# Performance work log

Hardware: AMD Instinct MI355X
Metric: run time of the kernel (lower is better)

Reference implementation:

```python
import jax, jax.numpy as jnp
import numpy as np

B = 64          # batch of puzzles
N = 16          # board_size
H = 128         # hidden_dim
S = 3           # msg_passing_steps
E = 131072      # edges per edge type
T = 5           # edge types: contains, lt, gt, may_contain, diff
NCELL = B * N * N          # 16384 cell nodes
NCLU = B * (N + 1)         # 1088 cluster nodes


def setup_inputs() -> dict:
    key = jax.random.key(0)
    ks = jax.random.split(key, 20)
    # edges[t] = (src, dst). Type 0 ('contains') sources from cluster nodes,
    # the rest are cell-to-cell. Destinations are always cell nodes.
    src0 = jax.random.randint(ks[0], (1, E), 0, NCLU)
    srcr = jax.random.randint(ks[1], (T - 1, E), 0, NCELL)
    src = jnp.concatenate([src0, srcr], axis=0)
    dst = jax.random.randint(ks[2], (T, E), 0, NCELL)
    edges = jnp.stack([src, dst], axis=1).astype(jnp.int32)  # [T,2,E]
    q = jax.random.randint(ks[3], (NCELL,), 0, N + 1).astype(jnp.int32)

    def lin(k, fan_in, shape):
        return (jax.random.normal(k, shape, dtype=jnp.float32) / np.sqrt(fan_in)).astype(jnp.float32)

    inp = {
        'edges': edges,
        'q': q,
        'input_embeddings': lin(ks[4], H, (NCLU, H)) * np.sqrt(H) * 0.1,
        'output_embeddings': lin(ks[5], H, (NCLU, H)) * np.sqrt(H) * 0.1,
        'mlp_W1': lin(ks[6], 2 * H, (T, 2 * H, H)),
        'mlp_b1': jnp.zeros((T, H), jnp.float32),
        'mlp_W2': lin(ks[7], H, (T, H, H)),
        'mlp_b2': jnp.zeros((T, H), jnp.float32),
        'mlp_W3': lin(ks[8], H, (T, H, H)),
        'mlp_b3': jnp.zeros((T, H), jnp.float32),
        'mlp_W4': lin(ks[9], H, (T, H, H)),
        'mlp_b4': jnp.zeros((T, H), jnp.float32),
        'lstm_Wih': lin(ks[10], (T + 1) * H, ((T + 1) * H, 4 * H)),
        'lstm_Whh': lin(ks[11], H, (H, 4 * H)),
    }
    return inp


def _forward(edges, q, input_embeddings, output_embeddings,
             mlp_W1, mlp_b1, mlp_W2, mlp_b2, mlp_W3, mlp_b3, mlp_W4, mlp_b4,
             lstm_Wih, lstm_Whh):
    cell_sno = jnp.arange(NCELL, dtype=jnp.int32) // (N * N)
    clu_sno = jnp.arange(NCLU, dtype=jnp.int32) // (N + 1)
    clu_id = jnp.arange(NCLU, dtype=jnp.int32) % (N + 1)

    # cluster input: embedding lookup at id + (N+1)*sno
    cluster_x = input_embeddings[clu_id + (N + 1) * clu_sno]  # [NCLU, H]

    # cell input: class-0 row replaced by mean of classes 1..N, then lookup by q
    emb = input_embeddings.reshape(B, N + 1, H)
    avg = emb[:, 1:, :].mean(axis=1, keepdims=True)
    lookup = jnp.concatenate([avg, emb[:, 1:, :]], axis=1).reshape(NCLU, H)
    cell_x = lookup[q + (N + 1) * cell_sno]  # [NCELL, H]

    h = cell_x
    rnn_h = jnp.zeros_like(cell_x)
    rnn_c = jnp.zeros_like(cell_x)
    h_clu = cluster_x  # cluster state held fixed across steps

    outs = []
    for _ in range(S):
        msgs = []
        for t in range(T):
            src, dst = edges[t, 0], edges[t, 1]
            hs = (h_clu if t == 0 else h)[src]   # gather source states
            hd = h[dst]                           # gather dest states
            z = jnp.concatenate([hs, hd], axis=-1)          # [E, 2H]
            z = jax.nn.relu(z @ mlp_W1[t] + mlp_b1[t])
            z = jax.nn.relu(z @ mlp_W2[t] + mlp_b2[t])
            z = jax.nn.relu(z @ mlp_W3[t] + mlp_b3[t])
            z = z @ mlp_W4[t] + mlp_b4[t]                   # final Linear, no ReLU
            msgs.append(jax.ops.segment_sum(z, dst, num_segments=NCELL))
        lstm_in = jnp.concatenate([cell_x] + msgs, axis=-1)  # [NCELL, (T+1)H]
        gates = lstm_in @ lstm_Wih + rnn_h @ lstm_Whh        # bias=False LSTMCell
        i, f, g, o = jnp.split(gates, 4, axis=-1)            # torch gate order
        rnn_c = jax.nn.sigmoid(f) * rnn_c + jax.nn.sigmoid(i) * jnp.tanh(g)
        rnn_h = jax.nn.sigmoid(o) * jnp.tanh(rnn_c)
        h = rnn_h
        outs.append(h)

    cell_outputs = jnp.stack(outs)  # [S, NCELL, H]
    # calc_logits: bilinear contraction of cell states with output class embeddings
    logits = jnp.einsum('sbnh,bch->sbnc',
                        cell_outputs.reshape(S, B, N * N, H),
                        output_embeddings.reshape(B, N + 1, H))
    return logits.reshape(S, B * N * N, N + 1)


def reference(edges, q, input_embeddings, output_embeddings,
              mlp_W1, mlp_b1, mlp_W2, mlp_b2, mlp_W3, mlp_b3, mlp_W4, mlp_b4,
              lstm_Wih, lstm_Whh):
    return _forward(edges, q, input_embeddings, output_embeddings,
                    mlp_W1, mlp_b1, mlp_W2, mlp_b2, mlp_W3, mlp_b3, mlp_W4, mlp_b4,
                    lstm_Wih, lstm_Whh)
```

## Files before the change

kernel.cpp:

```cpp
#include <hip/hip_runtime.h>
#include <hip/hip_fp16.h>
#include <math.h>

#define H 128
#define SSTEPS 3
#define NE 131072
#define NT 5
#define NCELL 16384
#define NCLU 1088
#define G4 512
#define MSGW 640
#define AKT 28
#define EB 128

typedef unsigned short u16;
typedef unsigned int u32;
typedef __attribute__((ext_vector_type(8))) short short8;
typedef __attribute__((ext_vector_type(8))) unsigned short ushort8;
typedef __attribute__((ext_vector_type(4))) unsigned short ushort4v;
typedef __attribute__((ext_vector_type(4))) float f32x4;

__device__ __forceinline__ u16 f2bf(float f) {
    unsigned int u = __float_as_uint(f);
    u += 0x7fffu + ((u >> 16) & 1u);
    return (u16)(u >> 16);
}
__device__ __forceinline__ float bf2f(u16 h) {
    return __uint_as_float(((unsigned int)h) << 16);
}

__global__ __launch_bounds__(128) void k_avg(const float* __restrict__ emb,
                                             float* __restrict__ avg) {
    int b = blockIdx.x, hc = threadIdx.x;
    float s = 0.f;
#pragma unroll
    for (int r = 1; r <= 16; ++r) s += emb[(b * 17 + r) * H + hc];
    avg[b * H + hc] = s * (1.0f / 16.0f);
}

__global__ __launch_bounds__(256) void k_init(const int* __restrict__ q,
                                              const float* __restrict__ emb,
                                              const float* __restrict__ avg,
                                              u16* __restrict__ Ap, size_t aplane,
                                              float* __restrict__ rnn_h,
                                              float* __restrict__ cst) {
    __shared__ float sx[16][132];
    int mtile = blockIdx.x, tid = threadIdx.x;
#pragma unroll
    for (int e = 0; e < 8; ++e) {
        int idx = e * 256 + tid;
        int row = idx >> 7, c = idx & 127;
        int grow = mtile * 16 + row;
        int b = grow >> 8;
        int qi = q[grow];
        const float* src = (qi == 0) ? (avg + b * H) : (emb + (b * 17 + qi) * H);
        float v = src[c];
        sx[row][c] = v;
        rnn_h[(size_t)grow * H + c] = 0.f;
        cst[(size_t)grow * H + c] = 0.f;
    }
    __syncthreads();
    int kt = tid >> 6, lane = tid & 63;
    int row = lane & 15, c0 = kt * 32 + ((lane >> 4) << 3);
    ushort8 hh, ll;
#pragma unroll
    for (int i = 0; i < 8; ++i) {
        float x = sx[row][c0 + i];
        u16 h = f2bf(x);
        hh[i] = h;
        ll[i] = f2bf(x - bf2f(h));
    }
    size_t fo = ((size_t)(mtile * AKT + kt) * 64 + lane) * 8;
    *reinterpret_cast<ushort8*>(Ap + fo) = hh;
    *reinterpret_cast<ushort8*>(Ap + aplane + fo) = ll;
}

__global__ __launch_bounds__(256) void k_zeromsg(__half* __restrict__ msg) {
    int idx = blockIdx.x * 256 + threadIdx.x;
    reinterpret_cast<float4*>(msg)[idx] = make_float4(0.f, 0.f, 0.f, 0.f);
}

__global__ __launch_bounds__(256) void k_gemm32(const float* __restrict__ A, int lda,
                                                const float* __restrict__ B, int ldb,
                                                u16* __restrict__ C, int ldc, int K) {
    __shared__ float As[64][33];
    __shared__ float Bs[32][64];
    int tid = threadIdx.x;
    int ty = tid >> 4, tx = tid & 15;
    int rbase = blockIdx.x * 64, cbase = blockIdx.y * 64;
    float acc[4][4] = {};
    for (int k0 = 0; k0 < K; k0 += 32) {
        __syncthreads();
#pragma unroll
        for (int i = 0; i < 8; ++i) {
            int id = tid + i * 256;
            int r = id >> 5, c = id & 31;
            As[r][c] = A[(size_t)(rbase + r) * lda + k0 + c];
        }
#pragma unroll
        for (int i = 0; i < 8; ++i) {
            int id = tid + i * 256;
            int r = id >> 6, c = id & 63;
            Bs[r][c] = B[(size_t)(k0 + r) * ldb + cbase + c];
        }
        __syncthreads();
#pragma unroll 8
        for (int kk = 0; kk < 32; ++kk) {
            float a[4], bv[4];
#pragma unroll
            for (int i = 0; i < 4; ++i) a[i] = As[ty * 4 + i][kk];
#pragma unroll
            for (int j = 0; j < 4; ++j) bv[j] = Bs[kk][tx * 4 + j];
#pragma unroll
            for (int i = 0; i < 4; ++i)
#pragma unroll
                for (int j = 0; j < 4; ++j) acc[i][j] = fmaf(a[i], bv[j], acc[i][j]);
        }
    }
#pragma unroll
    for (int i = 0; i < 4; ++i)
#pragma unroll
        for (int j = 0; j < 4; ++j)
            C[(size_t)(rbase + ty * 4 + i) * ldc + cbase + tx * 4 + j] = f2bf(acc[i][j]);
}

__global__ __launch_bounds__(256) void k_prepw(const float* __restrict__ W2,
                                               const float* __restrict__ W3,
                                               const float* __restrict__ W4,
                                               u16* __restrict__ WF) {
    int bid = blockIdx.x;
    int t = bid / 48;
    int l = (bid / 16) % 3;
    int p = (bid / 8) % 2;
    int nt = bid % 8;
    int tid = threadIdx.x;
    int ks = tid >> 6, lane = tid & 63;
    const float* W = (l == 0 ? W2 : l == 1 ? W3 : W4) + t * 16384;
    int n = nt * 16 + (lane & 15);
    int kb = ks * 32 + (lane >> 4) * 8;
    ushort8 o;
#pragma unroll
    for (int i = 0; i < 8; ++i) {
        float w = W[(size_t)(kb + i) * H + n];
        u16 h = f2bf(w);
        o[i] = (p == 0) ? h : f2bf(w - bf2f(h));
    }
    size_t base = ((size_t)((((t * 3 + l) * 2 + p) * 8 + nt) * 4 + ks) * 64 + lane) * 8;
    *reinterpret_cast<ushort8*>(WF + base) = o;
}

__global__ __launch_bounds__(256) void k_packBw(const float* __restrict__ Wih,
                                                const float* __restrict__ Whh,
                                                u16* __restrict__ Bw, size_t bplane) {
    int nt = blockIdx.x;
    int kt = blockIdx.y * 4 + (threadIdx.x >> 6);
    int lane = threadIdx.x & 63;
    int n = nt * 16 + (lane & 15);
    int k0 = kt * 32 + ((lane >> 4) << 3);
    ushort8 hh, ll;
#pragma unroll
    for (int i = 0; i < 8; ++i) {
        int k = k0 + i;
        float wv = (k < 768) ? Wih[(size_t)k * G4 + n] : Whh[(size_t)(k - 768) * G4 + n];
        u16 h = f2bf(wv);
        hh[i] = h;
        ll[i] = f2bf(wv - bf2f(h));
    }
    size_t fo = ((size_t)(nt * AKT + kt) * 64 + lane) * 8;
    *reinterpret_cast<ushort8*>(Bw + fo) = hh;
    *reinterpret_cast<ushort8*>(Bw + bplane + fo) = ll;
}

__global__ __launch_bounds__(256) void k_packBp(const float* __restrict__ W1,
                                                u16* __restrict__ Bp, size_t bplane) {
    int nt = blockIdx.x;
    int kt = threadIdx.x >> 6;
    int lane = threadIdx.x & 63;
    int n = nt * 16 + (lane & 15);
    int k0 = kt * 32 + ((lane >> 4) << 3);
    int t, roff, j;
    if (n < 640) { t = n >> 7; j = n & 127; roff = 128; }
    else { int m = n - 640; t = (m >> 7) + 1; j = m & 127; roff = 0; }
    ushort8 hh, ll;
#pragma unroll
    for (int i = 0; i < 8; ++i) {
        float wv = W1[((size_t)t * 256 + roff + k0 + i) * H + j];
        u16 h = f2bf(wv);
        hh[i] = h;
        ll[i] = f2bf(wv - bf2f(h));
    }
    size_t fo = ((size_t)(nt * 4 + kt) * 64 + lane) * 8;
    *reinterpret_cast<ushort8*>(Bp + fo) = hh;
    *reinterpret_cast<ushort8*>(Bp + bplane + fo) = ll;
}

__global__ __launch_bounds__(256) void k_packmsg(const __half* __restrict__ msg,
                                                 u16* __restrict__ Ap, size_t aplane) {
    int mtile = blockIdx.x;
    int ktl = blockIdx.y * 4 + (threadIdx.x >> 6);
    int lane = threadIdx.x & 63;
    int row = mtile * 16 + (lane & 15);
    int c0 = ktl * 32 + ((lane >> 4) << 3);
    const __half* mrow = msg + (size_t)row * MSGW;
    ushort8 hh, ll;
#pragma unroll
    for (int i = 0; i < 8; ++i) {
        int fg = c0 + i;
        int tt = fg >> 7, fl = fg & 127;
        int pos = tt * 128 + ((fl >> 5) << 5) + ((fl & 15) << 1) + ((fl >> 4) & 1);
        float x = __half2float(mrow[pos]);
        u16 h = f2bf(x);
        hh[i] = h;
        ll[i] = f2bf(x - bf2f(h));
    }
    size_t fo = ((size_t)(mtile * AKT + 4 + ktl) * 64 + lane) * 8;
    *reinterpret_cast<ushort8*>(Ap + fo) = hh;
    *reinterpret_cast<ushort8*>(Ap + aplane + fo) = ll;
}

__global__ __launch_bounds__(256) void k_gemm_bf(const u16* __restrict__ Ap, size_t aplane,
                                                 int aktbase,
                                                 const u16* __restrict__ Bp, size_t bplane,
                                                 int bKT, int nkt,
                                                 float* __restrict__ Cf, u16* __restrict__ Ch,
                                                 int ldc, int psplit) {
    int tid = threadIdx.x;
    int w = tid >> 6, lane = tid & 63;
    int wr = w >> 1, wc = w & 1;
    int mtb = blockIdx.x * 8 + wr * 4;
    int ntb = blockIdx.y * 8 + wc * 4;
    f32x4 acc[4][4] = {};
    for (int kk = 0; kk < nkt; ++kk) {
        short8 Ah[4], Al[4], Bh[4], Bl[4];
#pragma unroll
        for (int m = 0; m < 4; ++m) {
            size_t fo = ((size_t)((mtb + m) * AKT + aktbase + kk) * 64 + lane) * 8;
            Ah[m] = *reinterpret_cast<const short8*>(Ap + fo);
            Al[m] = *reinterpret_cast<const short8*>(Ap + aplane + fo);
        }
#pragma unroll
        for (int n = 0; n < 4; ++n) {
            size_t fo = ((size_t)((ntb + n) * bKT + kk) * 64 + lane) * 8;
            Bh[n] = *reinterpret_cast<const short8*>(Bp + fo);
            Bl[n] = *reinterpret_cast<const short8*>(Bp + bplane + fo);
        }
#pragma unroll
        for (int m = 0; m < 4; ++m)
#pragma unroll
            for (int n = 0; n < 4; ++n) {
                acc[m][n] = __builtin_amdgcn_mfma_f32_16x16x32_bf16(Ah[m], Bh[n], acc[m][n], 0, 0, 0);
                acc[m][n] = __builtin_amdgcn_mfma_f32_16x16x32_bf16(Ah[m], Bl[n], acc[m][n], 0, 0, 0);
                acc[m][n] = __builtin_amdgcn_mfma_f32_16x16x32_bf16(Al[m], Bh[n], acc[m][n], 0, 0, 0);
            }
    }
#pragma unroll
    for (int m = 0; m < 4; ++m)
#pragma unroll
        for (int r = 0; r < 4; ++r) {
            int row = (mtb + m) * 16 + (lane >> 4) * 4 + r;
#pragma unroll
            for (int n = 0; n < 4; ++n) {
                int col = (ntb + n) * 16 + (lane & 15);
                float v = acc[m][n][r];
                if (Ch) {
                    if (psplit)
                        Ch[((size_t)(col >> 7) * NCELL + row) * H + (col & 127)] = f2bf(v);
                    else
                        Ch[(size_t)row * ldc + col] = f2bf(v);
                } else {
                    Cf[(size_t)row * ldc + col] = v;
                }
            }
        }
}

__global__ __launch_bounds__(256, 4) void k_edge(const int* __restrict__ edges,
                                                 const u16* __restrict__ P,
                                                 const u16* __restrict__ Ps0,
                                                 const u16* __restrict__ WF,
                                                 const float* __restrict__ bb1,
                                                 const float* __restrict__ bb2,
                                                 const float* __restrict__ bb3,
                                                 const float* __restrict__ bb4,
                                                 __half* __restrict__ msg) {
    __shared__ u16 zh[EB * H];
    __shared__ int sdst[EB];
    int tid = threadIdx.x;
    int w = tid >> 6, lane = tid & 63;
    int bid = blockIdx.x;
    int t = bid >> 10, tile = bid & 1023;
    int ebase = tile * EB;

    {
        int row = tid >> 1, half = tid & 1;
        int e = ebase + row;
        int sn = edges[(t * 2) * NE + e];
        int dn = edges[(t * 2 + 1) * NE + e];
        if (half == 0) sdst[row] = dn;
        const u16* ps = (t == 0) ? Ps0 + (size_t)sn * H
                                 : P + ((size_t)(t + 4) * NCELL + sn) * H;
        const u16* pd = P + ((size_t)t * NCELL + dn) * H;
        const float* bb = bb1 + t * H;
#pragma unroll
        for (int cc = 0; cc < 8; ++cc) {
            int c8 = half * 8 + cc;
            ushort8 a = *reinterpret_cast<const ushort8*>(ps + c8 * 8);
            ushort8 d = *reinterpret_cast<const ushort8*>(pd + c8 * 8);
            float4 b0 = *reinterpret_cast<const float4*>(bb + c8 * 8);
            float4 b1v = *reinterpret_cast<const float4*>(bb + c8 * 8 + 4);
            float bv[8] = {b0.x, b0.y, b0.z, b0.w, b1v.x, b1v.y, b1v.z, b1v.w};
            ushort8 hh;
#pragma unroll
            for (int i = 0; i < 8; ++i)
                hh[i] = f2bf(fmaxf(bf2f(a[i]) + bf2f(d[i]) + bv[i], 0.f));
            *reinterpret_cast<ushort8*>(&zh[row * H + ((c8 ^ (row & 7)) << 3)]) = hh;
        }
    }
    __syncthreads();

    const u16* wfbase = WF + (size_t)(t * 3) * 32768;
    short8 Bh[2][4], Bl[2][4];

#pragma unroll 1
    for (int l = 0; l < 2; ++l) {
        const u16* wl = wfbase + l * 32768;
#pragma unroll
        for (int fg = 0; fg < 2; ++fg)
#pragma unroll
            for (int ks = 0; ks < 4; ++ks) {
                int nt = 2 * w + fg;
                Bh[fg][ks] = *reinterpret_cast<const short8*>(wl + ((nt * 4 + ks) * 64 + lane) * 8);
                Bl[fg][ks] = *reinterpret_cast<const short8*>(wl + ((32 + nt * 4 + ks) * 64 + lane) * 8);
            }
        f32x4 acc[8][2];
#pragma unroll
        for (int et = 0; et < 8; ++et)
#pragma unroll
            for (int fg = 0; fg < 2; ++fg)
                acc[et][fg] = (f32x4){0.f, 0.f, 0.f, 0.f};
#pragma unroll
        for (int et = 0; et < 8; ++et) {
            short8 Zf[4];
            int rr = et * 16 + (lane & 15);
#pragma unroll
            for (int ks = 0; ks < 4; ++ks) {
                int ch = ks * 4 + (lane >> 4);
                Zf[ks] = *reinterpret_cast<const short8*>(&zh[rr * H + ((ch ^ (rr & 7)) << 3)]);
            }
#pragma unroll
            for (int fg = 0; fg < 2; ++fg)
#pragma unroll
                for (int ks = 0; ks < 4; ++ks) {
                    acc[et][fg] = __builtin_amdgcn_mfma_f32_16x16x32_bf16(Bh[fg][ks], Zf[ks], acc[et][fg], 0, 0, 0);
                    acc[et][fg] = __builtin_amdgcn_mfma_f32_16x16x32_bf16(Bl[fg][ks], Zf[ks], acc[et][fg], 0, 0, 0);
                }
        }
        __syncthreads();
        const float* bb = (l == 0 ? bb2 : bb3) + t * H;
        float bi[2][4];
#pragma unroll
        for (int fg = 0; fg < 2; ++fg)
#pragma unroll
            for (int r = 0; r < 4; ++r)
                bi[fg][r] = bb[(2 * w + fg) * 16 + (lane >> 4) * 4 + r];
#pragma unroll
        for (int et = 0; et < 8; ++et) {
            int e = et * 16 + (lane & 15);
#pragma unroll
            for (int fg = 0; fg < 2; ++fg) {
                int f0 = (2 * w + fg) * 16 + (lane >> 4) * 4;
                ushort4v v;
#pragma unroll
                for (int r = 0; r < 4; ++r)
                    v[r] = f2bf(fmaxf(acc[et][fg][r] + bi[fg][r], 0.f));
                int off = e * H + (((f0 >> 3) ^ (e & 7)) << 3) + (f0 & 7);
                *reinterpret_cast<ushort4v*>(&zh[off]) = v;
            }
        }
        __syncthreads();
    }

    {
        const u16* wl = wfbase + 2 * 32768;
#pragma unroll
        for (int ng = 0; ng < 2; ++ng)
#pragma unroll
            for (int ks = 0; ks < 4; ++ks) {
                int nt = 2 * w + ng;
                Bh[ng][ks] = *reinterpret_cast<const short8*>(wl + ((nt * 4 + ks) * 64 + lane) * 8);
                Bl[ng][ks] = *reinterpret_cast<const short8*>(wl + ((32 + nt * 4 + ks) * 64 + lane) * 8);
            }
        const float* bb = bb4 + t * H;
        float bi[2];
#pragma unroll
        for (int ng = 0; ng < 2; ++ng) bi[ng] = bb[(2 * w + ng) * 16 + (lane & 15)];
        int pos = (w * 16 + (lane & 15)) * 2;
#pragma unroll 1
        for (int mt = 0; mt < 8; ++mt) {
            short8 Ah[4];
            int rr = mt * 16 + (lane & 15);
#pragma unroll
            for (int ks = 0; ks < 4; ++ks) {
                int ch = ks * 4 + (lane >> 4);
                Ah[ks] = *reinterpret_cast<const short8*>(&zh[rr * H + ((ch ^ (rr & 7)) << 3)]);
            }
            f32x4 a0 = (f32x4){0.f, 0.f, 0.f, 0.f};
            f32x4 a1 = (f32x4){0.f, 0.f, 0.f, 0.f};
#pragma unroll
            for (int ks = 0; ks < 4; ++ks) {
                a0 = __builtin_amdgcn_mfma_f32_16x16x32_bf16(Ah[ks], Bh[0][ks], a0, 0, 0, 0);
                a0 = __builtin_amdgcn_mfma_f32_16x16x32_bf16(Ah[ks], Bl[0][ks], a0, 0, 0, 0);
                a1 = __builtin_amdgcn_mfma_f32_16x16x32_bf16(Ah[ks], Bh[1][ks], a1, 0, 0, 0);
                a1 = __builtin_amdgcn_mfma_f32_16x16x32_bf16(Ah[ks], Bl[1][ks], a1, 0, 0, 0);
            }
#pragma unroll
            for (int r = 0; r < 4; ++r) {
                int d = sdst[mt * 16 + (lane >> 4) * 4 + r];
                __half2* mp = reinterpret_cast<__half2*>(msg + (size_t)d * MSGW + t * H + pos);
                unsafeAtomicAdd(mp, __floats2half2_rn(a0[r] + bi[0], a1[r] + bi[1]));
            }
        }
    }
}

__global__ __launch_bounds__(256) void k_lstm(const float* __restrict__ gates,
                                              float* __restrict__ cst,
                                              float* __restrict__ rnn_h,
                                              u16* __restrict__ Ap, size_t aplane) {
    __shared__ float sh[16][132];
    int mtile = blockIdx.x, tid = threadIdx.x;
#pragma unroll
    for (int e = 0; e < 8; ++e) {
        int idx = e * 256 + tid;
        int row = idx >> 7, c = idx & 127;
        int grow = mtile * 16 + row;
        const float* g = gates + (size_t)grow * G4;
        float ig = g[c], fg = g[128 + c], gg = g[256 + c], og = g[384 + c];
        size_t ci = (size_t)grow * H + c;
        float c_old = cst[ci];
        float i_s = 1.f / (1.f + expf(-ig));
        float f_s = 1.f / (1.f + expf(-fg));
        float o_s = 1.f / (1.f + expf(-og));
        float c_new = f_s * c_old + i_s * tanhf(gg);
        float h_new = o_s * tanhf(c_new);
        cst[ci] = c_new;
        rnn_h[ci] = h_new;
        sh[row][c] = h_new;
    }
    __syncthreads();
    int kt = tid >> 6, lane = tid & 63;
    int row = lane & 15, c0 = kt * 32 + ((lane >> 4) << 3);
    ushort8 hh, ll;
#pragma unroll
    for (int i = 0; i < 8; ++i) {
        float x = sh[row][c0 + i];
        u16 h = f2bf(x);
        hh[i] = h;
        ll[i] = f2bf(x - bf2f(h));
    }
    size_t fo = ((size_t)(mtile * AKT + 24 + kt) * 64 + lane) * 8;
    *reinterpret_cast<ushort8*>(Ap + fo) = hh;
    *reinterpret_cast<ushort8*>(Ap + aplane + fo) = ll;
}

__global__ __launch_bounds__(256) void k_logits(const float* __restrict__ h,
                                                const float* __restrict__ oemb,
                                                float* __restrict__ out) {
    __shared__ float oe[17][129];
    int b = blockIdx.x, tid = threadIdx.x;
    for (int id = tid; id < 17 * 128; id += 256) {
        int r = id >> 7, c = id & 127;
        oe[r][c] = oemb[(b * 17 + r) * H + c];
    }
    __syncthreads();
    const float* hr = h + (size_t)(b * 256 + tid) * H;
    float acc[17] = {};
    for (int v = 0; v < 32; ++v) {
        float4 hv = reinterpret_cast<const float4*>(hr)[v];
#pragma unroll
        for (int cls = 0; cls < 17; ++cls) {
            acc[cls] = fmaf(hv.x, oe[cls][v * 4 + 0],
                       fmaf(hv.y, oe[cls][v * 4 + 1],
                       fmaf(hv.z, oe[cls][v * 4 + 2],
                       fmaf(hv.w, oe[cls][v * 4 + 3], acc[cls]))));
        }
    }
    float* op = out + (size_t)(b * 256 + tid) * 17;
#pragma unroll
    for (int cls = 0; cls < 17; ++cls) op[cls] = acc[cls];
}

extern "C" void kernel_launch(void* const* d_in, const int* in_sizes, int n_in,
                              void* d_out, int out_size, void* d_ws, size_t ws_size,
                              hipStream_t stream) {
    (void)in_sizes; (void)n_in; (void)out_size; (void)ws_size;
    const int*   edges = (const int*)d_in[0];
    const int*   q     = (const int*)d_in[1];
    const float* emb   = (const float*)d_in[2];
    const float* oemb  = (const float*)d_in[3];
    const float* W1    = (const float*)d_in[4];
    const float* b1    = (const float*)d_in[5];
    const float* W2    = (const float*)d_in[6];
    const float* b2    = (const float*)d_in[7];
    const float* W3    = (const float*)d_in[8];
    const float* b3    = (const float*)d_in[9];
    const float* W4    = (const float*)d_in[10];
    const float* b4    = (const float*)d_in[11];
    const float* Wih   = (const float*)d_in[12];
    const float* Whh   = (const float*)d_in[13];
    float* out = (float*)d_out;

    char* wsp = (char*)d_ws;
    size_t off = 0;
    auto alloc = [&](size_t bytes) { void* p = wsp + off; off = (off + bytes + 255) & ~(size_t)255; return p; };
    __half* msg   = (__half*)alloc((size_t)NCELL * MSGW * 2);
    u16*   P      = (u16*)  alloc((size_t)9 * NCELL * H * 2);
    float* gates  = (float*)P;
    float* rnn_h  = (float*)alloc((size_t)NCELL * H * 4);
    float* cst    = (float*)alloc((size_t)NCELL * H * 4);
    u16*   Ps0    = (u16*)  alloc((size_t)NCLU * H * 2);
    float* avg    = (float*)alloc((size_t)64 * H * 4);
    size_t aplane = (size_t)NCELL * 896;
    u16*   Ap     = (u16*)  alloc(aplane * 2 * 2);
    u16*   WF     = (u16*)  alloc((size_t)983040 * 2);
    size_t bwpl   = (size_t)512 * 896;
    u16*   Bw     = (u16*)  alloc(bwpl * 2 * 2);
    size_t bppl   = (size_t)1152 * 128;
    u16*   Bp     = (u16*)  alloc(bppl * 2 * 2);

    k_avg<<<64, 128, 0, stream>>>(emb, avg);
    k_init<<<1024, 256, 0, stream>>>(q, emb, avg, Ap, aplane, rnn_h, cst);
    k_prepw<<<240, 256, 0, stream>>>(W2, W3, W4, WF);
    {
        dim3 g(32, 7);
        k_packBw<<<g, 256, 0, stream>>>(Wih, Whh, Bw, bwpl);
    }
    k_packBp<<<72, 256, 0, stream>>>(W1, Bp, bppl);
    {
        dim3 g0(17, 2);
        k_gemm32<<<g0, 256, 0, stream>>>(emb, H, W1, H, Ps0, H, H);
    }

    for (int s = 0; s < SSTEPS; ++s) {
        k_zeromsg<<<NCELL * MSGW / 8 / 256, 256, 0, stream>>>(msg);
        {
            dim3 g(128, 9);
            k_gemm_bf<<<g, 256, 0, stream>>>(Ap, aplane, (s == 0) ? 0 : 24,
                                             Bp, bppl, 4, 4, nullptr, P, H, 1);
        }
        k_edge<<<NT * (NE / EB), 256, 0, stream>>>(edges, P, Ps0, WF,
                                                   b1, b2, b3, b4, msg);
        {
            dim3 g(1024, 5);
            k_packmsg<<<g, 256, 0, stream>>>(msg, Ap, aplane);
        }
        {
            dim3 g(128, 4);
            k_gemm_bf<<<g, 256, 0, stream>>>(Ap, aplane, 0, Bw, bwpl, AKT,
                                             (s == 0) ? 24 : 28, gates, nullptr, G4, 0);
        }
        k_lstm<<<1024, 256, 0, stream>>>(gates, cst, rnn_h, Ap, aplane);
        k_logits<<<64, 256, 0, stream>>>(rnn_h, oemb, out + (size_t)s * NCELL * 17);
    }
}
```

Before: 1.150 ms.

## Fuse logits into LSTM kernel, halve edge tile, drop rnn_h buffer

The logits contraction moves into the LSTM kernel, so the new hidden state is read from shared memory instead of being written to and re-read from a global rnn_h buffer, and one launch per step goes away. The edge kernel tile shrinks from 128 to 64 edges with launch bounds raised to 8 blocks per CU, aiming for more occupancy and latency hiding, though each block's weight-fragment loads are now amortised over fewer edges. The bf16 conversion switches to the library intrinsic. Each LSTM block now reloads 17 output-embedding rows, which adds redundant global reads.

```diff
diff --git a/kernel.cpp b/kernel.cpp
--- a/kernel.cpp
+++ b/kernel.cpp
@@ -1,5 +1,6 @@
 #include <hip/hip_runtime.h>
 #include <hip/hip_fp16.h>
+#include <hip/hip_bf16.h>
 #include <math.h>
 
 #define H 128
@@ -11,7 +12,7 @@
 #define G4 512
 #define MSGW 640
 #define AKT 28
-#define EB 128
+#define EB 64
 
 typedef unsigned short u16;
 typedef unsigned int u32;
@@ -21,9 +22,10 @@
 typedef __attribute__((ext_vector_type(4))) float f32x4;
 
 __device__ __forceinline__ u16 f2bf(float f) {
-    unsigned int u = __float_as_uint(f);
-    u += 0x7fffu + ((u >> 16) & 1u);
-    return (u16)(u >> 16);
+    __hip_bfloat16 h = __float2bfloat16(f);
+    u16 u;
+    __builtin_memcpy(&u, &h, 2);
+    return u;
 }
 __device__ __forceinline__ float bf2f(u16 h) {
     return __uint_as_float(((unsigned int)h) << 16);
@@ -42,7 +44,6 @@
                                               const float* __restrict__ emb,
                                               const float* __restrict__ avg,
                                               u16* __restrict__ Ap, size_t aplane,
-                                              float* __restrict__ rnn_h,
                                               float* __restrict__ cst) {
     __shared__ float sx[16][132];
     int mtile = blockIdx.x, tid = threadIdx.x;
@@ -56,7 +57,6 @@
         const float* src = (qi == 0) ? (avg + b * H) : (emb + (b * 17 + qi) * H);
         float v = src[c];
         sx[row][c] = v;
-        rnn_h[(size_t)grow * H + c] = 0.f;
         cst[(size_t)grow * H + c] = 0.f;
     }
     __syncthreads();
@@ -274,7 +274,7 @@
         }
 }
 
-__global__ __launch_bounds__(256, 4) void k_edge(const int* __restrict__ edges,
+__global__ __launch_bounds__(256, 8) void k_edge(const int* __restrict__ edges,
                                                  const u16* __restrict__ P,
                                                  const u16* __restrict__ Ps0,
                                                  const u16* __restrict__ WF,
@@ -288,22 +288,22 @@
     int tid = threadIdx.x;
     int w = tid >> 6, lane = tid & 63;
     int bid = blockIdx.x;
-    int t = bid >> 10, tile = bid & 1023;
+    int t = bid >> 11, tile = bid & 2047;
     int ebase = tile * EB;
 
     {
-        int row = tid >> 1, half = tid & 1;
+        int row = tid >> 2, quar = tid & 3;
         int e = ebase + row;
         int sn = edges[(t * 2) * NE + e];
         int dn = edges[(t * 2 + 1) * NE + e];
-        if (half == 0) sdst[row] = dn;
+        if (quar == 0) sdst[row] = dn;
         const u16* ps = (t == 0) ? Ps0 + (size_t)sn * H
                                  : P + ((size_t)(t + 4) * NCELL + sn) * H;
         const u16* pd = P + ((size_t)t * NCELL + dn) * H;
         const float* bb = bb1 + t * H;
 #pragma unroll
-        for (int cc = 0; cc < 8; ++cc) {
-            int c8 = half * 8 + cc;
+        for (int cc = 0; cc < 4; ++cc) {
+            int c8 = quar * 4 + cc;
             ushort8 a = *reinterpret_cast<const ushort8*>(ps + c8 * 8);
             ushort8 d = *reinterpret_cast<const ushort8*>(pd + c8 * 8);
             float4 b0 = *reinterpret_cast<const float4*>(bb + c8 * 8);
@@ -332,14 +332,14 @@
                 Bh[fg][ks] = *reinterpret_cast<const short8*>(wl + ((nt * 4 + ks) * 64 + lane) * 8);
                 Bl[fg][ks] = *reinterpret_cast<const short8*>(wl + ((32 + nt * 4 + ks) * 64 + lane) * 8);
             }
-        f32x4 acc[8][2];
-#pragma unroll
-        for (int et = 0; et < 8; ++et)
+        f32x4 acc[4][2];
+#pragma unroll
+        for (int et = 0; et < 4; ++et)
 #pragma unroll
             for (int fg = 0; fg < 2; ++fg)
                 acc[et][fg] = (f32x4){0.f, 0.f, 0.f, 0.f};
 #pragma unroll
-        for (int et = 0; et < 8; ++et) {
+        for (int et = 0; et < 4; ++et) {
             short8 Zf[4];
             int rr = et * 16 + (lane & 15);
 #pragma unroll
@@ -364,7 +364,7 @@
             for (int r = 0; r < 4; ++r)
                 bi[fg][r] = bb[(2 * w + fg) * 16 + (lane >> 4) * 4 + r];
 #pragma unroll
-        for (int et = 0; et < 8; ++et) {
+        for (int et = 0; et < 4; ++et) {
             int e = et * 16 + (lane & 15);
 #pragma unroll
             for (int fg = 0; fg < 2; ++fg) {
@@ -396,7 +396,7 @@
         for (int ng = 0; ng < 2; ++ng) bi[ng] = bb[(2 * w + ng) * 16 + (lane & 15)];
         int pos = (w * 16 + (lane & 15)) * 2;
 #pragma unroll 1
-        for (int mt = 0; mt < 8; ++mt) {
+        for (int mt = 0; mt < 4; ++mt) {
             short8 Ah[4];
             int rr = mt * 16 + (lane & 15);
 #pragma unroll
@@ -425,10 +425,17 @@
 
 __global__ __launch_bounds__(256) void k_lstm(const float* __restrict__ gates,
                                               float* __restrict__ cst,
-                                              float* __restrict__ rnn_h,
-                                              u16* __restrict__ Ap, size_t aplane) {
+                                              u16* __restrict__ Ap, size_t aplane,
+                                              const float* __restrict__ oemb,
+                                              float* __restrict__ out) {
     __shared__ float sh[16][132];
+    __shared__ float oe[17][132];
     int mtile = blockIdx.x, tid = threadIdx.x;
+    int b = mtile >> 4;
+    for (int id = tid; id < 17 * 128; id += 256) {
+        int r = id >> 7, c = id & 127;
+        oe[r][c] = oemb[(b * 17 + r) * H + c];
+    }
 #pragma unroll
     for (int e = 0; e < 8; ++e) {
         int idx = e * 256 + tid;
@@ -444,50 +451,47 @@
         float c_new = f_s * c_old + i_s * tanhf(gg);
         float h_new = o_s * tanhf(c_new);
         cst[ci] = c_new;
-        rnn_h[ci] = h_new;
         sh[row][c] = h_new;
     }
     __syncthreads();
-    int kt = tid >> 6, lane = tid & 63;
-    int row = lane & 15, c0 = kt * 32 + ((lane >> 4) << 3);
-    ushort8 hh, ll;
-#pragma unroll
-    for (int i = 0; i < 8; ++i) {
-        float x = sh[row][c0 + i];
-        u16 h = f2bf(x);
-        hh[i] = h;
-        ll[i] = f2bf(x - bf2f(h));
-    }
-    size_t fo = ((size_t)(mtile * AKT + 24 + kt) * 64 + lane) * 8;
-    *reinterpret_cast<ushort8*>(Ap + fo) = hh;
-    *reinterpret_cast<ushort8*>(Ap + aplane + fo) = ll;
-}
-
-__global__ __launch_bounds__(256) void k_logits(const float* __restrict__ h,
-                                                const float* __restrict__ oemb,
-                                                float* __restrict__ out) {
-    __shared__ float oe[17][129];
-    int b = blockIdx.x, tid = threadIdx.x;
-    for (int id = tid; id < 17 * 128; id += 256) {
-        int r = id >> 7, c = id & 127;
-        oe[r][c] = oemb[(b * 17 + r) * H + c];
-    }
-    __syncthreads();
-    const float* hr = h + (size_t)(b * 256 + tid) * H;
-    float acc[17] = {};
-    for (int v = 0; v < 32; ++v) {
-        float4 hv = reinterpret_cast<const float4*>(hr)[v];
-#pragma unroll
-        for (int cls = 0; cls < 17; ++cls) {
-            acc[cls] = fmaf(hv.x, oe[cls][v * 4 + 0],
-                       fmaf(hv.y, oe[cls][v * 4 + 1],
-                       fmaf(hv.z, oe[cls][v * 4 + 2],
-                       fmaf(hv.w, oe[cls][v * 4 + 3], acc[cls]))));
-        }
-    }
-    float* op = out + (size_t)(b * 256 + tid) * 17;
-#pragma unroll
-    for (int cls = 0; cls < 17; ++cls) op[cls] = acc[cls];
+    {
+        int kt = tid >> 6, lane = tid & 63;
+        int row = lane & 15, c0 = kt * 32 + ((lane >> 4) << 3);
+        ushort8 hh, ll;
+#pragma unroll
+        for (int i = 0; i < 8; ++i) {
+            float x = sh[row][c0 + i];
+            u16 h = f2bf(x);
+            hh[i] = h;
+            ll[i] = f2bf(x - bf2f(h));
+        }
+        size_t fo = ((size_t)(mtile * AKT + 24 + kt) * 64 + lane) * 8;
+        *reinterpret_cast<ushort8*>(Ap + fo) = hh;
+        *reinterpret_cast<ushort8*>(Ap + aplane + fo) = ll;
+    }
+    {
+        int row = tid & 15, cls = tid >> 4;
+        const float4* hv = reinterpret_cast<const float4*>(&sh[row][0]);
+        const float4* ov = reinterpret_cast<const float4*>(&oe[cls][0]);
+        float a = 0.f;
+#pragma unroll
+        for (int v = 0; v < 32; ++v) {
+            float4 h4 = hv[v], o4 = ov[v];
+            a = fmaf(h4.x, o4.x, fmaf(h4.y, o4.y, fmaf(h4.z, o4.z, fmaf(h4.w, o4.w, a))));
+        }
+        out[(size_t)(mtile * 16 + row) * 17 + cls] = a;
+        if (tid < 16) {
+            const float4* hv2 = reinterpret_cast<const float4*>(&sh[tid][0]);
+            const float4* ov2 = reinterpret_cast<const float4*>(&oe[16][0]);
+            float a2 = 0.f;
+#pragma unroll
+            for (int v = 0; v < 32; ++v) {
+                float4 h4 = hv2[v], o4 = ov2[v];
+                a2 = fmaf(h4.x, o4.x, fmaf(h4.y, o4.y, fmaf(h4.z, o4.z, fmaf(h4.w, o4.w, a2))));
+            }
+            out[(size_t)(mtile * 16 + tid) * 17 + 16] = a2;
+        }
+    }
 }
 
 extern "C" void kernel_launch(void* const* d_in, const int* in_sizes, int n_in,
@@ -516,7 +520,6 @@
     __half* msg   = (__half*)alloc((size_t)NCELL * MSGW * 2);
     u16*   P      = (u16*)  alloc((size_t)9 * NCELL * H * 2);
     float* gates  = (float*)P;
-    float* rnn_h  = (float*)alloc((size_t)NCELL * H * 4);
     float* cst    = (float*)alloc((size_t)NCELL * H * 4);
     u16*   Ps0    = (u16*)  alloc((size_t)NCLU * H * 2);
     float* avg    = (float*)alloc((size_t)64 * H * 4);
@@ -529,7 +532,7 @@
     u16*   Bp     = (u16*)  alloc(bppl * 2 * 2);
 
     k_avg<<<64, 128, 0, stream>>>(emb, avg);
-    k_init<<<1024, 256, 0, stream>>>(q, emb, avg, Ap, aplane, rnn_h, cst);
+    k_init<<<1024, 256, 0, stream>>>(q, emb, avg, Ap, aplane, cst);
     k_prepw<<<240, 256, 0, stream>>>(W2, W3, W4, WF);
     {
         dim3 g(32, 7);
@@ -559,7 +562,7 @@
             k_gemm_bf<<<g, 256, 0, stream>>>(Ap, aplane, 0, Bw, bwpl, AKT,
                                              (s == 0) ? 24 : 28, gates, nullptr, G4, 0);
         }
-        k_lstm<<<1024, 256, 0, stream>>>(gates, cst, rnn_h, Ap, aplane);
-        k_logits<<<64, 256, 0, stream>>>(rnn_h, oemb, out + (size_t)s * NCELL * 17);
-    }
-}
+        k_lstm<<<1024, 256, 0, stream>>>(gates, cst, Ap, aplane, oemb,
+                                         out + (size_t)s * NCELL * 17);
+    }
+}
```

After: 1.439 ms. +25.1%, slower.
